# Optimization experiments

Measured on AMD Instinct MI355X. Metric: run time of the kernel, lower is better.

## Reference

```python
import jax, jax.numpy as jnp
import numpy as np

B, H, W, C, UNITS = 16, 64, 64, 64, 128

def setup_inputs() -> dict:
    key = jax.random.key(0)
    k1, k2 = jax.random.split(key)
    x = jax.random.normal(k1, (B, H, W, C), dtype=jnp.float32)
    # 'random_normal' keras initializer defaults to stddev=0.05
    w = jax.random.normal(k2, (UNITS, C, W, H), dtype=jnp.float32) * 0.05
    return {"x": x, "w": w}

def reference(x, w):
    # Original: transpose NHWC->NCHW, broadcasted matmul (W,H)@(H,W),
    # reduce-sum over C, transpose back, relu.
    # Fused contraction: y[b,i,j,u] = sum_{c,h} w[u,c,i,h] * x[b,h,j,c]
    y = jnp.einsum('ucih,bhjc->biju', w, x)  # (B, W, W, units)
    return jax.nn.relu(y)
```

## Files before the change

### kernel.cpp

```cpp
#include <hip/hip_runtime.h>
#include <hip/hip_bf16.h>


typedef __attribute__((ext_vector_type(4))) float f32x4;
typedef __attribute__((ext_vector_type(8))) short bf16x8;
typedef __attribute__((ext_vector_type(4))) unsigned int u32x4;
typedef __attribute__((ext_vector_type(2))) unsigned int u32x2;
typedef unsigned short ushort_t;

static __device__ __forceinline__ unsigned int cvt_pk_bf16(float lo, float hi) {
  unsigned int r;
  asm("v_cvt_pk_bf16_f32 %0, %1, %2" : "=v"(r) : "v"(lo), "v"(hi));
  return r;
}

static __device__ __forceinline__ void async_copy16(void* lds, const void* g) {
  __builtin_amdgcn_global_load_lds(
      (const __attribute__((address_space(1))) unsigned int*)g,
      (__attribute__((address_space(3))) unsigned int*)lds, 16, 0, 0);
}

__global__ __launch_bounds__(256)
void conv_x(const float* __restrict__ X, ushort_t* __restrict__ Xb, int n4) {
  int idx = blockIdx.x * 256 + threadIdx.x;
  const int stride = gridDim.x * 256;
  for (; idx < n4; idx += stride) {
    f32x4 v = ((const f32x4*)X)[idx];
    u32x2 o;
    o.x = cvt_pk_bf16(v.x, v.y);
    o.y = cvt_pk_bf16(v.z, v.w);
    ((u32x2*)Xb)[idx] = o;
  }
}

__global__ __launch_bounds__(256)
void conv_w(const float* __restrict__ W, ushort_t* __restrict__ Wb) {
  __shared__ float T[64][65];
  const int bid = blockIdx.x;
  const int u = bid >> 6;
  const int i = bid & 63;
  const int t = threadIdx.x;

  const int hq = t & 15;
  const int c4 = t >> 4;
  const float* base = W + (((size_t)u * 64) * 64 + i) * 64;
#pragma unroll
  for (int it = 0; it < 4; ++it) {
    const int c = it * 16 + c4;
    f32x4 v = *(const f32x4*)(base + (size_t)c * 4096 + hq * 4);
    *(f32x4*)&T[c][hq * 4] = v;
  }
  __syncthreads();

  const int h = t >> 2;
  const int c0 = (t & 3) * 16;
  unsigned int pk[8];
#pragma unroll
  for (int q = 0; q < 8; ++q)
    pk[q] = cvt_pk_bf16(T[c0 + 2 * q][h], T[c0 + 2 * q + 1][h]);
  ushort_t* out = Wb + (((size_t)i * 128 + u) * 64 + h) * 64 + c0;
  ((u32x4*)out)[0] = *(u32x4*)&pk[0];
  ((u32x4*)out)[1] = *(u32x4*)&pk[4];
}

__global__ __launch_bounds__(512, 2)
void gemm8(const ushort_t* __restrict__ Xb, const ushort_t* __restrict__ Wb,
           float* __restrict__ O) {
  __shared__ ushort_t As[3][128 * 64];
  __shared__ ushort_t Bs[3][256 * 64];

  const int tid = threadIdx.x;
  const int lane = tid & 63;
  const int wid = tid >> 6;
  const int wm = wid >> 2;
  const int wn = wid & 3;

  const int bid = blockIdx.x;
  const int wg = (bid & 7) * 32 + (bid >> 3);
  const int mt = wg & 7;
  const int nt2 = wg >> 3;

  const char* XbB = (const char*)Xb;
  const char* WbB = (const char*)Wb;

  int a_dst[2]; size_t a_src[2];
#pragma unroll
  for (int it = 0; it < 2; ++it) {
    const int flat = it * 8192 + tid * 16;
    const int row = flat >> 7;
    const int p = (flat >> 4) & 7;
    const int b = mt * 2 + (row >> 6);
    const int j = row & 63;
    a_dst[it] = flat;
    a_src[it] = (size_t)b * 524288 + (size_t)j * 128 + ((p ^ (row & 7)) << 4);
  }
  int b_dst[4]; size_t b_src[4];
#pragma unroll
  for (int it = 0; it < 4; ++it) {
    const int flat = it * 8192 + tid * 16;
    const int nl = flat >> 7;
    const int p = (flat >> 4) & 7;
    b_dst[it] = flat;
    b_src[it] = (size_t)(nt2 * 256 + nl) * 8192 + ((p ^ (nl & 7)) << 4);
  }

  int a_ro[2][4], b_ro[2][4];
#pragma unroll
  for (int kk = 0; kk < 2; ++kk) {
#pragma unroll
    for (int f = 0; f < 4; ++f) {
      int row = wm * 64 + f * 16 + (lane & 15);
      int byte0 = row * 128 + kk * 64 + (lane >> 4) * 16;
      a_ro[kk][f] = byte0 ^ ((row & 7) << 4);
      row = wn * 64 + f * 16 + (lane & 15);
      byte0 = row * 128 + kk * 64 + (lane >> 4) * 16;
      b_ro[kk][f] = byte0 ^ ((row & 7) << 4);
    }
  }

  f32x4 acc[4][4];
#pragma unroll
  for (int i = 0; i < 4; ++i)
#pragma unroll
    for (int j = 0; j < 4; ++j) acc[i][j] = (f32x4){0.f, 0.f, 0.f, 0.f};

  auto stage = [&](int buf, int h) {
    char* la = (char*)&As[buf][0];
    char* lb = (char*)&Bs[buf][0];
#pragma unroll
    for (int it = 0; it < 2; ++it)
      async_copy16(la + a_dst[it], XbB + a_src[it] + (size_t)h * 8192);
#pragma unroll
    for (int it = 0; it < 4; ++it)
      async_copy16(lb + b_dst[it], WbB + b_src[it] + (size_t)h * 128);
  };
  auto stage3a = [&](int buf, int h) {
    char* la = (char*)&As[buf][0];
    char* lb = (char*)&Bs[buf][0];
#pragma unroll
    for (int it = 0; it < 2; ++it)
      async_copy16(la + a_dst[it], XbB + a_src[it] + (size_t)h * 8192);
    async_copy16(lb + b_dst[0], WbB + b_src[0] + (size_t)h * 128);
  };
  auto stage3b = [&](int buf, int h) {
    char* lb = (char*)&Bs[buf][0];
#pragma unroll
    for (int it = 1; it < 4; ++it)
      async_copy16(lb + b_dst[it], WbB + b_src[it] + (size_t)h * 128);
  };

  bf16x8 fa0[4], fb0[4], fa1[4], fb1[4];

  auto readFrags = [&](bf16x8 (&fa)[4], bf16x8 (&fb)[4], int buf, int kk) {
    const char* ab = (const char*)&As[buf][0];
    const char* bb = (const char*)&Bs[buf][0];
#pragma unroll
    for (int f = 0; f < 4; ++f) fa[f] = *(const bf16x8*)(ab + a_ro[kk][f]);
#pragma unroll
    for (int f = 0; f < 4; ++f) fb[f] = *(const bf16x8*)(bb + b_ro[kk][f]);
  };

  stage(0, 0);
  stage(1, 1);
  asm volatile("s_waitcnt vmcnt(6)" ::: "memory");
  __builtin_amdgcn_s_barrier();
  readFrags(fa0, fb0, 0, 0);

  int cur = 0, nxt = 1, pre = 2;
  for (int t = 0; t < 64; ++t) {
    __builtin_amdgcn_sched_barrier(0);
    readFrags(fa1, fb1, cur, 1);
    if (t + 2 < 64) stage3a(pre, t + 2);
    if (t < 62) {
      asm volatile("s_waitcnt vmcnt(3)" ::: "memory");
    } else {
      asm volatile("s_waitcnt vmcnt(0)" ::: "memory");
    }
    __builtin_amdgcn_sched_barrier(0);
    __builtin_amdgcn_s_barrier();
    __builtin_amdgcn_s_setprio(1);
#pragma unroll
    for (int mf = 0; mf < 4; ++mf)
#pragma unroll
      for (int nf = 0; nf < 4; ++nf)
        acc[mf][nf] = __builtin_amdgcn_mfma_f32_16x16x32_bf16(
            fa0[mf], fb0[nf], acc[mf][nf], 0, 0, 0);
    __builtin_amdgcn_s_setprio(0);
    __builtin_amdgcn_s_barrier();

    __builtin_amdgcn_sched_barrier(0);
    if (t + 1 < 64) readFrags(fa0, fb0, nxt, 0);
    if (t + 2 < 64) stage3b(pre, t + 2);
    __builtin_amdgcn_sched_barrier(0);
    __builtin_amdgcn_s_barrier();
    __builtin_amdgcn_s_setprio(1);
#pragma unroll
    for (int mf = 0; mf < 4; ++mf)
#pragma unroll
      for (int nf = 0; nf < 4; ++nf)
        acc[mf][nf] = __builtin_amdgcn_mfma_f32_16x16x32_bf16(
            fa1[mf], fb1[nf], acc[mf][nf], 0, 0, 0);
    __builtin_amdgcn_s_setprio(0);
    __builtin_amdgcn_s_barrier();

    cur = (cur == 2) ? 0 : cur + 1;
    nxt = (nxt == 2) ? 0 : nxt + 1;
    pre = (pre == 2) ? 0 : pre + 1;
  }

  const int rbase = (lane >> 4) * 4;
  const int cn = lane & 15;
#pragma unroll
  for (int mf = 0; mf < 4; ++mf) {
#pragma unroll
    for (int r = 0; r < 4; ++r) {
      const int ml = wm * 64 + mf * 16 + rbase + r;
      const int m = mt * 128 + ml;
      const int b = m >> 6;
      const int j = m & 63;
#pragma unroll
      for (int nf = 0; nf < 4; ++nf) {
        const int nloc = wn * 64 + nf * 16 + cn;
        const int i = nt2 * 2 + (nloc >> 7);
        const int u = nloc & 127;
        O[(((size_t)b * 64 + i) * 64 + j) * 128 + u] = fmaxf(acc[mf][nf][r], 0.f);
      }
    }
  }
}

__global__ __launch_bounds__(256, 2)
void fused_gemm(const float* __restrict__ X, const float* __restrict__ Wt,
                float* __restrict__ O) {
  __shared__ ushort_t As[2][128 * 64];
  __shared__ ushort_t Bs[2][128 * 64];
  const int tid = threadIdx.x;
  const int lane = tid & 63;
  const int wid = tid >> 6;
  const int wm = wid >> 1;
  const int wn = wid & 1;
  const int bid = blockIdx.x;
  const int wg = (bid & 7) * 64 + (bid >> 3);
  const int mt = wg & 7;
  const int nt = wg >> 3;
  const int a_ml = tid >> 1;
  const int a_hp = (tid & 1) * 2;
  const int a_b = (mt * 128 + a_ml) >> 6;
  const int a_j = a_ml & 63;
  const float* a_base = X + ((size_t)a_b << 18) + ((size_t)a_j << 6);
  const int b_nl = tid >> 1;
  const int b_c8 = (tid & 1) * 8;
  const float* b_base = Wt + ((size_t)b_nl << 18) + ((size_t)nt << 6);
  f32x4 ra[2][4];
  f32x4 rb[8];
  f32x4 acc[4][4];
#pragma unroll
  for (int i = 0; i < 4; ++i)
#pragma unroll
    for (int j = 0; j < 4; ++j) acc[i][j] = (f32x4){0.f, 0.f, 0.f, 0.f};
  auto stage_load = [&](int t) {
    const int th = t & 15;
    const int tc = t >> 4;
    const int c0 = tc * 16;
    const int h0 = th * 4;
#pragma unroll
    for (int s = 0; s < 2; ++s) {
      const float* p = a_base + (size_t)(h0 + a_hp + s) * 4096 + c0;
#pragma unroll
      for (int q = 0; q < 4; ++q) ra[s][q] = ((const f32x4*)p)[q];
    }
#pragma unroll
    for (int q = 0; q < 8; ++q)
      rb[q] = *(const f32x4*)(b_base + (size_t)(c0 + b_c8 + q) * 4096 + h0);
  };
  auto stage_write = [&](int buf) {
    char* abase = (char*)&As[buf][0];
    const int swa = (a_ml & 7) << 4;
#pragma unroll
    for (int s = 0; s < 2; ++s) {
      u32x4 lo, hi;
      lo.x = cvt_pk_bf16(ra[s][0].x, ra[s][0].y);
      lo.y = cvt_pk_bf16(ra[s][0].z, ra[s][0].w);
      lo.z = cvt_pk_bf16(ra[s][1].x, ra[s][1].y);
      lo.w = cvt_pk_bf16(ra[s][1].z, ra[s][1].w);
      hi.x = cvt_pk_bf16(ra[s][2].x, ra[s][2].y);
      hi.y = cvt_pk_bf16(ra[s][2].z, ra[s][2].w);
      hi.z = cvt_pk_bf16(ra[s][3].x, ra[s][3].y);
      hi.w = cvt_pk_bf16(ra[s][3].z, ra[s][3].w);
      const int byte0 = a_ml * 128 + (a_hp + s) * 32;
      *(u32x4*)(abase + (byte0 ^ swa)) = lo;
      *(u32x4*)(abase + ((byte0 + 16) ^ swa)) = hi;
    }
    char* bbase = (char*)&Bs[buf][0];
    const int swb = (b_nl & 7) << 4;
#pragma unroll
    for (int hl = 0; hl < 4; ++hl) {
      u32x4 v;
      v.x = cvt_pk_bf16(rb[0][hl], rb[1][hl]);
      v.y = cvt_pk_bf16(rb[2][hl], rb[3][hl]);
      v.z = cvt_pk_bf16(rb[4][hl], rb[5][hl]);
      v.w = cvt_pk_bf16(rb[6][hl], rb[7][hl]);
      const int byte0 = b_nl * 128 + (hl * 16 + b_c8) * 2;
      *(u32x4*)(bbase + (byte0 ^ swb)) = v;
    }
  };
  auto compute = [&](int buf) {
    const char* abase = (const char*)&As[buf][0];
    const char* bbase = (const char*)&Bs[buf][0];
#pragma unroll
    for (int kk = 0; kk < 2; ++kk) {
      bf16x8 af[4], bfr[4];
#pragma unroll
      for (int mf = 0; mf < 4; ++mf) {
        const int row = wm * 64 + mf * 16 + (lane & 15);
        const int byte0 = row * 128 + kk * 64 + (lane >> 4) * 16;
        af[mf] = *(const bf16x8*)(abase + (byte0 ^ ((row & 7) << 4)));
      }
#pragma unroll
      for (int nf = 0; nf < 4; ++nf) {
        const int row = wn * 64 + nf * 16 + (lane & 15);
        const int byte0 = row * 128 + kk * 64 + (lane >> 4) * 16;
        bfr[nf] = *(const bf16x8*)(bbase + (byte0 ^ ((row & 7) << 4)));
      }
#pragma unroll
      for (int mf = 0; mf < 4; ++mf)
#pragma unroll
        for (int nf = 0; nf < 4; ++nf)
          acc[mf][nf] = __builtin_amdgcn_mfma_f32_16x16x32_bf16(
              af[mf], bfr[nf], acc[mf][nf], 0, 0, 0);
    }
  };
  stage_load(0);
  stage_write(0);
  __syncthreads();
  int cur = 0;
  for (int t = 0; t < 64; ++t) {
    if (t + 1 < 64) stage_load(t + 1);
    compute(cur);
    if (t + 1 < 64) stage_write(cur ^ 1);
    __syncthreads();
    cur ^= 1;
  }
  const int rbase = (lane >> 4) * 4;
  const int cn = lane & 15;
#pragma unroll
  for (int mf = 0; mf < 4; ++mf) {
#pragma unroll
    for (int r = 0; r < 4; ++r) {
      const int ml = wm * 64 + mf * 16 + rbase + r;
      const int m = mt * 128 + ml;
      const int b = m >> 6;
      const int j = m & 63;
      float* orow = O + (((size_t)b * 64 + nt) * 64 + j) * 128;
#pragma unroll
      for (int nf = 0; nf < 4; ++nf) {
        const int u = wn * 64 + nf * 16 + cn;
        orow[u] = fmaxf(acc[mf][nf][r], 0.f);
      }
    }
  }
}

extern "C" void kernel_launch(void* const* d_in, const int* in_sizes, int n_in,
                              void* d_out, int out_size, void* d_ws, size_t ws_size,
                              hipStream_t stream) {
  const float* x = (const float*)d_in[0];
  const float* w = (const float*)d_in[1];
  float* out = (float*)d_out;

  const size_t XB_BYTES = (size_t)16 * 64 * 64 * 64 * 2;
  const size_t WB_BYTES = (size_t)64 * 128 * 64 * 64 * 2;

  if (ws_size >= XB_BYTES + WB_BYTES) {
    ushort_t* Xb = (ushort_t*)d_ws;
    ushort_t* Wb = (ushort_t*)((char*)d_ws + XB_BYTES);
    hipLaunchKernelGGL(conv_x, dim3(1024), dim3(256), 0, stream, x, Xb,
                       (int)(16 * 64 * 64 * 64 / 4));
    hipLaunchKernelGGL(conv_w, dim3(8192), dim3(256), 0, stream, w, Wb);
    hipLaunchKernelGGL(gemm8, dim3(256), dim3(512), 0, stream, Xb, Wb, out);
  } else {
    hipLaunchKernelGGL(fused_gemm, dim3(512), dim3(256), 0, stream, x, w, out);
  }
}
```

Before: 107.1 us.

## Replace 8-wave GEMM with 4-wave 256x128 tile kernel using fewer barriers

The main GEMM now uses 256-thread blocks of 4 waves. Each wave computes a 128x64 output tile (8x4 MFMA fragments) instead of 64x64, and the block tile changes from 128x256 to 256x128. This doubles per-wave register reuse of B fragments and removes two of the four s_barriers per K iteration, cutting LDS traffic per MFMA and sync overhead. In exchange it uses more accumulator registers, gives one block per CU, and has fewer waves to hide latency. Removing barriers between reading a buffer and refilling it may also risk LDS hazards.

```diff
diff --git a/kernel.cpp b/kernel.cpp
--- a/kernel.cpp
+++ b/kernel.cpp
@@ -63,33 +63,33 @@
   ((u32x4*)out)[1] = *(u32x4*)&pk[4];
 }
 
-__global__ __launch_bounds__(512, 2)
-void gemm8(const ushort_t* __restrict__ Xb, const ushort_t* __restrict__ Wb,
-           float* __restrict__ O) {
-  __shared__ ushort_t As[3][128 * 64];
-  __shared__ ushort_t Bs[3][256 * 64];
+__global__ __launch_bounds__(256, 1)
+void gemm4f(const ushort_t* __restrict__ Xb, const ushort_t* __restrict__ Wb,
+            float* __restrict__ O) {
+  __shared__ ushort_t As[3][256 * 64];
+  __shared__ ushort_t Bs[3][128 * 64];
 
   const int tid = threadIdx.x;
   const int lane = tid & 63;
   const int wid = tid >> 6;
-  const int wm = wid >> 2;
-  const int wn = wid & 3;
+  const int wm = wid >> 1;
+  const int wn = wid & 1;
 
   const int bid = blockIdx.x;
   const int wg = (bid & 7) * 32 + (bid >> 3);
-  const int mt = wg & 7;
-  const int nt2 = wg >> 3;
+  const int mt = wg & 3;
+  const int nt = wg >> 2;
 
   const char* XbB = (const char*)Xb;
   const char* WbB = (const char*)Wb;
 
-  int a_dst[2]; size_t a_src[2];
-#pragma unroll
-  for (int it = 0; it < 2; ++it) {
-    const int flat = it * 8192 + tid * 16;
+  int a_dst[8]; size_t a_src[8];
+#pragma unroll
+  for (int it = 0; it < 8; ++it) {
+    const int flat = it * 4096 + tid * 16;
     const int row = flat >> 7;
     const int p = (flat >> 4) & 7;
-    const int b = mt * 2 + (row >> 6);
+    const int b = mt * 4 + (row >> 6);
     const int j = row & 63;
     a_dst[it] = flat;
     a_src[it] = (size_t)b * 524288 + (size_t)j * 128 + ((p ^ (row & 7)) << 4);
@@ -97,72 +97,63 @@
   int b_dst[4]; size_t b_src[4];
 #pragma unroll
   for (int it = 0; it < 4; ++it) {
-    const int flat = it * 8192 + tid * 16;
-    const int nl = flat >> 7;
+    const int flat = it * 4096 + tid * 16;
+    const int u = flat >> 7;
     const int p = (flat >> 4) & 7;
     b_dst[it] = flat;
-    b_src[it] = (size_t)(nt2 * 256 + nl) * 8192 + ((p ^ (nl & 7)) << 4);
-  }
-
-  int a_ro[2][4], b_ro[2][4];
+    b_src[it] = (size_t)(nt * 128 + u) * 8192 + ((p ^ (u & 7)) << 4);
+  }
+
+  int a_ro[2][8], b_ro[2][4];
 #pragma unroll
   for (int kk = 0; kk < 2; ++kk) {
 #pragma unroll
+    for (int f = 0; f < 8; ++f) {
+      const int row = wm * 128 + f * 16 + (lane & 15);
+      const int byte0 = row * 128 + kk * 64 + (lane >> 4) * 16;
+      a_ro[kk][f] = byte0 ^ ((row & 7) << 4);
+    }
+#pragma unroll
     for (int f = 0; f < 4; ++f) {
-      int row = wm * 64 + f * 16 + (lane & 15);
-      int byte0 = row * 128 + kk * 64 + (lane >> 4) * 16;
-      a_ro[kk][f] = byte0 ^ ((row & 7) << 4);
-      row = wn * 64 + f * 16 + (lane & 15);
-      byte0 = row * 128 + kk * 64 + (lane >> 4) * 16;
+      const int row = wn * 64 + f * 16 + (lane & 15);
+      const int byte0 = row * 128 + kk * 64 + (lane >> 4) * 16;
       b_ro[kk][f] = byte0 ^ ((row & 7) << 4);
     }
   }
 
-  f32x4 acc[4][4];
-#pragma unroll
-  for (int i = 0; i < 4; ++i)
+  f32x4 acc[8][4];
+#pragma unroll
+  for (int i = 0; i < 8; ++i)
 #pragma unroll
     for (int j = 0; j < 4; ++j) acc[i][j] = (f32x4){0.f, 0.f, 0.f, 0.f};
 
-  auto stage = [&](int buf, int h) {
+  auto stageA = [&](int buf, int h) {
     char* la = (char*)&As[buf][0];
+#pragma unroll
+    for (int it = 0; it < 8; ++it)
+      async_copy16(la + a_dst[it], XbB + a_src[it] + (size_t)h * 8192);
+  };
+  auto stageB = [&](int buf, int h) {
     char* lb = (char*)&Bs[buf][0];
-#pragma unroll
-    for (int it = 0; it < 2; ++it)
-      async_copy16(la + a_dst[it], XbB + a_src[it] + (size_t)h * 8192);
 #pragma unroll
     for (int it = 0; it < 4; ++it)
       async_copy16(lb + b_dst[it], WbB + b_src[it] + (size_t)h * 128);
   };
-  auto stage3a = [&](int buf, int h) {
-    char* la = (char*)&As[buf][0];
-    char* lb = (char*)&Bs[buf][0];
-#pragma unroll
-    for (int it = 0; it < 2; ++it)
-      async_copy16(la + a_dst[it], XbB + a_src[it] + (size_t)h * 8192);
-    async_copy16(lb + b_dst[0], WbB + b_src[0] + (size_t)h * 128);
-  };
-  auto stage3b = [&](int buf, int h) {
-    char* lb = (char*)&Bs[buf][0];
-#pragma unroll
-    for (int it = 1; it < 4; ++it)
-      async_copy16(lb + b_dst[it], WbB + b_src[it] + (size_t)h * 128);
-  };
-
-  bf16x8 fa0[4], fb0[4], fa1[4], fb1[4];
-
-  auto readFrags = [&](bf16x8 (&fa)[4], bf16x8 (&fb)[4], int buf, int kk) {
+
+  bf16x8 fa0[8], fb0[4], fa1[8], fb1[4];
+
+  auto readFrags = [&](bf16x8 (&fa)[8], bf16x8 (&fb)[4], int buf, int kk) {
     const char* ab = (const char*)&As[buf][0];
     const char* bb = (const char*)&Bs[buf][0];
 #pragma unroll
-    for (int f = 0; f < 4; ++f) fa[f] = *(const bf16x8*)(ab + a_ro[kk][f]);
+    for (int f = 0; f < 8; ++f) fa[f] = *(const bf16x8*)(ab + a_ro[kk][f]);
 #pragma unroll
     for (int f = 0; f < 4; ++f) fb[f] = *(const bf16x8*)(bb + b_ro[kk][f]);
   };
 
-  stage(0, 0);
-  stage(1, 1);
-  asm volatile("s_waitcnt vmcnt(6)" ::: "memory");
+  stageA(0, 0); stageB(0, 0);
+  stageA(1, 1); stageB(1, 1);
+  asm volatile("s_waitcnt vmcnt(12)" ::: "memory");
   __builtin_amdgcn_s_barrier();
   readFrags(fa0, fb0, 0, 0);
 
@@ -170,9 +161,9 @@
   for (int t = 0; t < 64; ++t) {
     __builtin_amdgcn_sched_barrier(0);
     readFrags(fa1, fb1, cur, 1);
-    if (t + 2 < 64) stage3a(pre, t + 2);
+    if (t + 2 < 64) stageA(pre, t + 2);
     if (t < 62) {
-      asm volatile("s_waitcnt vmcnt(3)" ::: "memory");
+      asm volatile("s_waitcnt vmcnt(8)" ::: "memory");
     } else {
       asm volatile("s_waitcnt vmcnt(0)" ::: "memory");
     }
@@ -180,22 +171,19 @@
     __builtin_amdgcn_s_barrier();
     __builtin_amdgcn_s_setprio(1);
 #pragma unroll
-    for (int mf = 0; mf < 4; ++mf)
+    for (int mf = 0; mf < 8; ++mf)
 #pragma unroll
       for (int nf = 0; nf < 4; ++nf)
         acc[mf][nf] = __builtin_amdgcn_mfma_f32_16x16x32_bf16(
             fa0[mf], fb0[nf], acc[mf][nf], 0, 0, 0);
     __builtin_amdgcn_s_setprio(0);
-    __builtin_amdgcn_s_barrier();
 
     __builtin_amdgcn_sched_barrier(0);
     if (t + 1 < 64) readFrags(fa0, fb0, nxt, 0);
-    if (t + 2 < 64) stage3b(pre, t + 2);
-    __builtin_amdgcn_sched_barrier(0);
-    __builtin_amdgcn_s_barrier();
+    if (t + 2 < 64) stageB(pre, t + 2);
     __builtin_amdgcn_s_setprio(1);
 #pragma unroll
-    for (int mf = 0; mf < 4; ++mf)
+    for (int mf = 0; mf < 8; ++mf)
 #pragma unroll
       for (int nf = 0; nf < 4; ++nf)
         acc[mf][nf] = __builtin_amdgcn_mfma_f32_16x16x32_bf16(
@@ -211,19 +199,18 @@
   const int rbase = (lane >> 4) * 4;
   const int cn = lane & 15;
 #pragma unroll
-  for (int mf = 0; mf < 4; ++mf) {
+  for (int mf = 0; mf < 8; ++mf) {
 #pragma unroll
     for (int r = 0; r < 4; ++r) {
-      const int ml = wm * 64 + mf * 16 + rbase + r;
-      const int m = mt * 128 + ml;
+      const int ml = wm * 128 + mf * 16 + rbase + r;
+      const int m = mt * 256 + ml;
       const int b = m >> 6;
       const int j = m & 63;
+      float* orow = O + (((size_t)b * 64 + nt) * 64 + j) * 128;
 #pragma unroll
       for (int nf = 0; nf < 4; ++nf) {
-        const int nloc = wn * 64 + nf * 16 + cn;
-        const int i = nt2 * 2 + (nloc >> 7);
-        const int u = nloc & 127;
-        O[(((size_t)b * 64 + i) * 64 + j) * 128 + u] = fmaxf(acc[mf][nf][r], 0.f);
+        const int u = wn * 64 + nf * 16 + cn;
+        orow[u] = fmaxf(acc[mf][nf][r], 0.f);
       }
     }
   }
@@ -377,7 +364,7 @@
     hipLaunchKernelGGL(conv_x, dim3(1024), dim3(256), 0, stream, x, Xb,
                        (int)(16 * 64 * 64 * 64 / 4));
     hipLaunchKernelGGL(conv_w, dim3(8192), dim3(256), 0, stream, w, Wb);
-    hipLaunchKernelGGL(gemm8, dim3(256), dim3(512), 0, stream, Xb, Wb, out);
+    hipLaunchKernelGGL(gemm4f, dim3(256), dim3(256), 0, stream, Xb, Wb, out);
   } else {
     hipLaunchKernelGGL(fused_gemm, dim3(512), dim3(256), 0, stream, x, w, out);
   }
```

Result: slower. 148.0 us (+38.2%).

## Add split-K 256x256-tile GEMM with partial buffers and separate add+ReLU pass

Applied to the files above, without the earlier changes.

Adds a new GEMM kernel with 256x256 output tiles that splits the K dimension (h) in two, so each of the 256 workgroups handles half the reduction. The two halves go to the output buffer and a workspace buffer, and a separate add_relu kernel then sums them and applies ReLU. The larger tile raises operand reuse per LDS byte, and the K split keeps enough workgroups in flight. In exchange the fp32 partial result is written twice and read back, which adds memory traffic, an extra launch, and a larger workspace requirement.

```diff
diff --git a/kernel.cpp b/kernel.cpp
--- a/kernel.cpp
+++ b/kernel.cpp
@@ -63,6 +63,172 @@
   ((u32x4*)out)[1] = *(u32x4*)&pk[4];
 }
 
+__global__ __launch_bounds__(512, 1)
+void gemm256(const ushort_t* __restrict__ Xb, const ushort_t* __restrict__ Wb,
+             float* __restrict__ P0, float* __restrict__ P1) {
+  __shared__ ushort_t As[3][256 * 32];
+  __shared__ ushort_t Bs[3][256 * 32];
+
+  const int tid = threadIdx.x;
+  const int lane = tid & 63;
+  const int wid = tid >> 6;
+  const int wm = wid >> 2;
+  const int wn = wid & 3;
+
+  const int bid = blockIdx.x;
+  const int wg = (bid & 7) * 32 + (bid >> 3);
+  const int mt = wg & 3;
+  const int rest = wg >> 2;
+  const int ks = rest & 1;
+  const int nt2 = rest >> 1;
+
+  const char* XbB = (const char*)Xb;
+  const char* WbB = (const char*)Wb;
+  const int kb6 = ks * 32;
+
+  int a_dst[2]; size_t a_srcb[2];
+  int b_dst[2]; size_t b_srcb[2];
+#pragma unroll
+  for (int it = 0; it < 2; ++it) {
+    const int flat = it * 8192 + tid * 16;
+    const int row = flat >> 6;
+    const int p = (flat >> 4) & 3;
+    const int ps = p ^ ((row >> 1) & 3);
+    a_dst[it] = flat;
+    a_srcb[it] = (size_t)(mt * 4 + (row >> 6)) * 524288 +
+                 (size_t)(row & 63) * 128 + ps * 16;
+    b_dst[it] = flat;
+    b_srcb[it] = (size_t)(nt2 * 256 + row) * 8192 + ps * 16;
+  }
+
+  int a_ro[2][4], b_ro[4];
+#pragma unroll
+  for (int mh = 0; mh < 2; ++mh)
+#pragma unroll
+    for (int f = 0; f < 4; ++f) {
+      const int row = wm * 128 + mh * 64 + f * 16 + (lane & 15);
+      a_ro[mh][f] = row * 64 + (((lane >> 4) ^ ((row >> 1) & 3)) << 4);
+    }
+#pragma unroll
+  for (int f = 0; f < 4; ++f) {
+    const int row = wn * 64 + f * 16 + (lane & 15);
+    b_ro[f] = row * 64 + (((lane >> 4) ^ ((row >> 1) & 3)) << 4);
+  }
+
+  f32x4 acc[8][4];
+#pragma unroll
+  for (int i = 0; i < 8; ++i)
+#pragma unroll
+    for (int j = 0; j < 4; ++j) acc[i][j] = (f32x4){0.f, 0.f, 0.f, 0.f};
+
+  auto stageA = [&](int buf, int T) {
+    char* la = (char*)&As[buf][0];
+    const size_t koff = (size_t)(kb6 + (T >> 1)) * 8192 + (T & 1) * 64;
+#pragma unroll
+    for (int it = 0; it < 2; ++it)
+      async_copy16(la + a_dst[it], XbB + a_srcb[it] + koff);
+  };
+  auto stageB = [&](int buf, int T) {
+    char* lb = (char*)&Bs[buf][0];
+    const size_t koff = (size_t)(kb6 + (T >> 1)) * 128 + (T & 1) * 64;
+#pragma unroll
+    for (int it = 0; it < 2; ++it)
+      async_copy16(lb + b_dst[it], WbB + b_srcb[it] + koff);
+  };
+
+  stageA(0, 0); stageB(0, 0);
+  stageA(1, 1); stageB(1, 1);
+  asm volatile("s_waitcnt vmcnt(4)" ::: "memory");
+  __builtin_amdgcn_s_barrier();
+
+  int cur = 0, pre = 2;
+  for (int t = 0; t < 64; ++t) {
+    const char* ab = (const char*)&As[cur][0];
+    const char* bb = (const char*)&Bs[cur][0];
+    bf16x8 fa[4], fb[4], fa2[4];
+
+    __builtin_amdgcn_sched_barrier(0);
+#pragma unroll
+    for (int f = 0; f < 4; ++f) fa[f] = *(const bf16x8*)(ab + a_ro[0][f]);
+#pragma unroll
+    for (int f = 0; f < 4; ++f) fb[f] = *(const bf16x8*)(bb + b_ro[f]);
+    if (t + 2 < 64) stageA(pre, t + 2);
+    __builtin_amdgcn_s_barrier();
+    asm volatile("s_waitcnt lgkmcnt(0)" ::: "memory");
+    __builtin_amdgcn_sched_barrier(0);
+    __builtin_amdgcn_s_setprio(1);
+#pragma unroll
+    for (int f = 0; f < 4; ++f)
+#pragma unroll
+      for (int nf = 0; nf < 4; ++nf)
+        acc[f][nf] = __builtin_amdgcn_mfma_f32_16x16x32_bf16(
+            fa[f], fb[nf], acc[f][nf], 0, 0, 0);
+    __builtin_amdgcn_s_setprio(0);
+    __builtin_amdgcn_s_barrier();
+
+    __builtin_amdgcn_sched_barrier(0);
+#pragma unroll
+    for (int f = 0; f < 4; ++f) fa2[f] = *(const bf16x8*)(ab + a_ro[1][f]);
+    if (t + 2 < 64) stageB(pre, t + 2);
+    __builtin_amdgcn_s_barrier();
+    asm volatile("s_waitcnt lgkmcnt(0)" ::: "memory");
+    __builtin_amdgcn_sched_barrier(0);
+    __builtin_amdgcn_s_setprio(1);
+#pragma unroll
+    for (int f = 0; f < 4; ++f)
+#pragma unroll
+      for (int nf = 0; nf < 4; ++nf)
+        acc[4 + f][nf] = __builtin_amdgcn_mfma_f32_16x16x32_bf16(
+            fa2[f], fb[nf], acc[4 + f][nf], 0, 0, 0);
+    __builtin_amdgcn_s_setprio(0);
+    if (t < 62) {
+      asm volatile("s_waitcnt vmcnt(4)" ::: "memory");
+    } else if (t == 62) {
+      asm volatile("s_waitcnt vmcnt(0)" ::: "memory");
+    }
+    __builtin_amdgcn_s_barrier();
+
+    cur = (cur == 2) ? 0 : cur + 1;
+    pre = (pre == 2) ? 0 : pre + 1;
+  }
+
+  float* P = ks ? P1 : P0;
+  const int rbase = (lane >> 4) * 4;
+  const int cn = lane & 15;
+#pragma unroll
+  for (int mf = 0; mf < 8; ++mf) {
+#pragma unroll
+    for (int r = 0; r < 4; ++r) {
+      const int m = mt * 256 + wm * 128 + mf * 16 + rbase + r;
+      const int b = m >> 6;
+      const int j = m & 63;
+#pragma unroll
+      for (int nf = 0; nf < 4; ++nf) {
+        const int nloc = wn * 64 + nf * 16 + cn;
+        const int i = nt2 * 2 + (nloc >> 7);
+        const int u = nloc & 127;
+        P[(((size_t)b * 64 + i) * 64 + j) * 128 + u] = acc[mf][nf][r];
+      }
+    }
+  }
+}
+
+__global__ __launch_bounds__(256)
+void add_relu(float* __restrict__ Out, const float* __restrict__ P1, int n4) {
+  int idx = blockIdx.x * 256 + threadIdx.x;
+  const int stride = gridDim.x * 256;
+  for (; idx < n4; idx += stride) {
+    f32x4 a = ((const f32x4*)Out)[idx];
+    f32x4 b = ((const f32x4*)P1)[idx];
+    f32x4 r;
+    r.x = fmaxf(a.x + b.x, 0.f);
+    r.y = fmaxf(a.y + b.y, 0.f);
+    r.z = fmaxf(a.z + b.z, 0.f);
+    r.w = fmaxf(a.w + b.w, 0.f);
+    ((f32x4*)Out)[idx] = r;
+  }
+}
+
 __global__ __launch_bounds__(512, 2)
 void gemm8(const ushort_t* __restrict__ Xb, const ushort_t* __restrict__ Wb,
            float* __restrict__ O) {
@@ -150,7 +316,6 @@
   };
 
   bf16x8 fa0[4], fb0[4], fa1[4], fb1[4];
-
   auto readFrags = [&](bf16x8 (&fa)[4], bf16x8 (&fb)[4], int buf, int kk) {
     const char* ab = (const char*)&As[buf][0];
     const char* bb = (const char*)&Bs[buf][0];
@@ -370,8 +535,19 @@
 
   const size_t XB_BYTES = (size_t)16 * 64 * 64 * 64 * 2;
   const size_t WB_BYTES = (size_t)64 * 128 * 64 * 64 * 2;
-
-  if (ws_size >= XB_BYTES + WB_BYTES) {
+  const size_t P1_BYTES = (size_t)16 * 64 * 64 * 128 * 4;
+
+  if (ws_size >= XB_BYTES + WB_BYTES + P1_BYTES) {
+    ushort_t* Xb = (ushort_t*)d_ws;
+    ushort_t* Wb = (ushort_t*)((char*)d_ws + XB_BYTES);
+    float* P1 = (float*)((char*)d_ws + XB_BYTES + WB_BYTES);
+    hipLaunchKernelGGL(conv_x, dim3(1024), dim3(256), 0, stream, x, Xb,
+                       (int)(16 * 64 * 64 * 64 / 4));
+    hipLaunchKernelGGL(conv_w, dim3(8192), dim3(256), 0, stream, w, Wb);
+    hipLaunchKernelGGL(gemm256, dim3(256), dim3(512), 0, stream, Xb, Wb, out, P1);
+    hipLaunchKernelGGL(add_relu, dim3(2048), dim3(256), 0, stream, out, P1,
+                       (int)(16 * 64 * 64 * 128 / 4));
+  } else if (ws_size >= XB_BYTES + WB_BYTES) {
     ushort_t* Xb = (ushort_t*)d_ws;
     ushort_t* Wb = (ushort_t*)((char*)d_ws + XB_BYTES);
     hipLaunchKernelGGL(conv_x, dim3(1024), dim3(256), 0, stream, x, Xb,
```

After: 132.0 us. 23.2% more time.

## Fuse weight bf16 conversion into GEMM and transpose X to k-contiguous layout

Applied to the files above, without the earlier changes.

Removes the separate conv_w pre-pass. The GEMM now loads fp32 weights straight from global memory into registers, converts them to bf16 and writes them into LDS one stage ahead, with a software pipeline across two register sets. conv_x becomes a transpose kernel that lays X out so the GEMM's k dimension is contiguous. This avoids writing and re-reading a full bf16 copy of W, at the cost of register-staged loads instead of async LDS copies, extra VGPR pressure (launch bounds drop to one block per CU), and strided 32-byte fp32 reads of W.

```diff
diff --git a/kernel.cpp b/kernel.cpp
--- a/kernel.cpp
+++ b/kernel.cpp
@@ -5,7 +5,6 @@
 typedef __attribute__((ext_vector_type(4))) float f32x4;
 typedef __attribute__((ext_vector_type(8))) short bf16x8;
 typedef __attribute__((ext_vector_type(4))) unsigned int u32x4;
-typedef __attribute__((ext_vector_type(2))) unsigned int u32x2;
 typedef unsigned short ushort_t;
 
 static __device__ __forceinline__ unsigned int cvt_pk_bf16(float lo, float hi) {
@@ -21,51 +20,40 @@
 }
 
 __global__ __launch_bounds__(256)
-void conv_x(const float* __restrict__ X, ushort_t* __restrict__ Xb, int n4) {
-  int idx = blockIdx.x * 256 + threadIdx.x;
-  const int stride = gridDim.x * 256;
-  for (; idx < n4; idx += stride) {
-    f32x4 v = ((const f32x4*)X)[idx];
-    u32x2 o;
-    o.x = cvt_pk_bf16(v.x, v.y);
-    o.y = cvt_pk_bf16(v.z, v.w);
-    ((u32x2*)Xb)[idx] = o;
-  }
-}
-
-__global__ __launch_bounds__(256)
-void conv_w(const float* __restrict__ W, ushort_t* __restrict__ Wb) {
-  __shared__ float T[64][65];
+void conv_xT(const float* __restrict__ X, ushort_t* __restrict__ Xb) {
+  __shared__ float T[64][68];
   const int bid = blockIdx.x;
-  const int u = bid >> 6;
-  const int i = bid & 63;
+  const int b = bid >> 6;
+  const int j = bid & 63;
   const int t = threadIdx.x;
 
-  const int hq = t & 15;
-  const int c4 = t >> 4;
-  const float* base = W + (((size_t)u * 64) * 64 + i) * 64;
-#pragma unroll
-  for (int it = 0; it < 4; ++it) {
-    const int c = it * 16 + c4;
-    f32x4 v = *(const f32x4*)(base + (size_t)c * 4096 + hq * 4);
-    *(f32x4*)&T[c][hq * 4] = v;
+  {
+    const int h = t >> 2;
+    const int cq = (t & 3) * 16;
+    const float* src = X + (((size_t)(b * 64 + h) * 64 + j) * 64) + cq;
+#pragma unroll
+    for (int k = 0; k < 4; ++k) {
+      f32x4 v = ((const f32x4*)src)[k];
+      *(f32x4*)&T[h][cq + 4 * k] = v;
+    }
   }
   __syncthreads();
-
-  const int h = t >> 2;
-  const int c0 = (t & 3) * 16;
-  unsigned int pk[8];
-#pragma unroll
-  for (int q = 0; q < 8; ++q)
-    pk[q] = cvt_pk_bf16(T[c0 + 2 * q][h], T[c0 + 2 * q + 1][h]);
-  ushort_t* out = Wb + (((size_t)i * 128 + u) * 64 + h) * 64 + c0;
-  ((u32x4*)out)[0] = *(u32x4*)&pk[0];
-  ((u32x4*)out)[1] = *(u32x4*)&pk[4];
-}
-
-__global__ __launch_bounds__(512, 2)
-void gemm8(const ushort_t* __restrict__ Xb, const ushort_t* __restrict__ Wb,
-           float* __restrict__ O) {
+  {
+    const int c = t >> 2;
+    const int hq = (t & 3) * 16;
+    unsigned int pk[8];
+#pragma unroll
+    for (int k = 0; k < 8; ++k)
+      pk[k] = cvt_pk_bf16(T[hq + 2 * k][c], T[hq + 2 * k + 1][c]);
+    ushort_t* out = Xb + ((size_t)bid * 64 + c) * 64 + hq;
+    ((u32x4*)out)[0] = *(u32x4*)&pk[0];
+    ((u32x4*)out)[1] = *(u32x4*)&pk[4];
+  }
+}
+
+__global__ __launch_bounds__(512, 1)
+void gemm_fw(const ushort_t* __restrict__ Xb, const float* __restrict__ W,
+             float* __restrict__ O) {
   __shared__ ushort_t As[3][128 * 64];
   __shared__ ushort_t Bs[3][256 * 64];
 
@@ -81,27 +69,30 @@
   const int nt2 = wg >> 3;
 
   const char* XbB = (const char*)Xb;
-  const char* WbB = (const char*)Wb;
-
-  int a_dst[2]; size_t a_src[2];
+  const char* WB = (const char*)W;
+
+  int a_dst[2]; size_t a_gsrc[2];
 #pragma unroll
   for (int it = 0; it < 2; ++it) {
     const int flat = it * 8192 + tid * 16;
-    const int row = flat >> 7;
+    const int ml = flat >> 7;
     const int p = (flat >> 4) & 7;
-    const int b = mt * 2 + (row >> 6);
-    const int j = row & 63;
+    const int ps = p ^ (ml & 7);
     a_dst[it] = flat;
-    a_src[it] = (size_t)b * 524288 + (size_t)j * 128 + ((p ^ (row & 7)) << 4);
-  }
-  int b_dst[4]; size_t b_src[4];
-#pragma unroll
-  for (int it = 0; it < 4; ++it) {
-    const int flat = it * 8192 + tid * 16;
+    a_gsrc[it] = (size_t)(mt * 128 + ml) * 8192 + ps * 16;
+  }
+
+  int b_ldst[4]; size_t b_gsrc[4];
+#pragma unroll
+  for (int q = 0; q < 4; ++q) {
+    const int flat = q * 8192 + tid * 16;
     const int nl = flat >> 7;
     const int p = (flat >> 4) & 7;
-    b_dst[it] = flat;
-    b_src[it] = (size_t)(nt2 * 256 + nl) * 8192 + ((p ^ (nl & 7)) << 4);
+    const int ps = p ^ (nl & 7);
+    const int u = nl & 127;
+    const int il = nl >> 7;
+    b_ldst[q] = flat;
+    b_gsrc[q] = (size_t)u * 1048576 + (size_t)(nt2 * 2 + il) * 256 + ps * 32;
   }
 
   int a_ro[2][4], b_ro[2][4];
@@ -124,33 +115,34 @@
 #pragma unroll
     for (int j = 0; j < 4; ++j) acc[i][j] = (f32x4){0.f, 0.f, 0.f, 0.f};
 
-  auto stage = [&](int buf, int h) {
+  auto issueA = [&](int buf, int c) {
     char* la = (char*)&As[buf][0];
+#pragma unroll
+    for (int it = 0; it < 2; ++it)
+      async_copy16(la + a_dst[it], XbB + a_gsrc[it] + (size_t)c * 128);
+  };
+  auto issueB = [&](f32x4 (&r)[4][2], int c) {
+#pragma unroll
+    for (int q = 0; q < 4; ++q) {
+      const char* s = WB + b_gsrc[q] + (size_t)c * 16384;
+      r[q][0] = *(const f32x4*)s;
+      r[q][1] = *(const f32x4*)(s + 16);
+    }
+  };
+  auto cvtWriteB = [&](f32x4 (&r)[4][2], int buf) {
     char* lb = (char*)&Bs[buf][0];
 #pragma unroll
-    for (int it = 0; it < 2; ++it)
-      async_copy16(la + a_dst[it], XbB + a_src[it] + (size_t)h * 8192);
-#pragma unroll
-    for (int it = 0; it < 4; ++it)
-      async_copy16(lb + b_dst[it], WbB + b_src[it] + (size_t)h * 128);
-  };
-  auto stage3a = [&](int buf, int h) {
-    char* la = (char*)&As[buf][0];
-    char* lb = (char*)&Bs[buf][0];
-#pragma unroll
-    for (int it = 0; it < 2; ++it)
-      async_copy16(la + a_dst[it], XbB + a_src[it] + (size_t)h * 8192);
-    async_copy16(lb + b_dst[0], WbB + b_src[0] + (size_t)h * 128);
-  };
-  auto stage3b = [&](int buf, int h) {
-    char* lb = (char*)&Bs[buf][0];
-#pragma unroll
-    for (int it = 1; it < 4; ++it)
-      async_copy16(lb + b_dst[it], WbB + b_src[it] + (size_t)h * 128);
+    for (int q = 0; q < 4; ++q) {
+      u32x4 v;
+      v.x = cvt_pk_bf16(r[q][0].x, r[q][0].y);
+      v.y = cvt_pk_bf16(r[q][0].z, r[q][0].w);
+      v.z = cvt_pk_bf16(r[q][1].x, r[q][1].y);
+      v.w = cvt_pk_bf16(r[q][1].z, r[q][1].w);
+      *(u32x4*)(lb + b_ldst[q]) = v;
+    }
   };
 
   bf16x8 fa0[4], fb0[4], fa1[4], fb1[4];
-
   auto readFrags = [&](bf16x8 (&fa)[4], bf16x8 (&fb)[4], int buf, int kk) {
     const char* ab = (const char*)&As[buf][0];
     const char* bb = (const char*)&Bs[buf][0];
@@ -160,23 +152,21 @@
     for (int f = 0; f < 4; ++f) fb[f] = *(const bf16x8*)(bb + b_ro[kk][f]);
   };
 
-  stage(0, 0);
-  stage(1, 1);
-  asm volatile("s_waitcnt vmcnt(6)" ::: "memory");
-  __builtin_amdgcn_s_barrier();
-  readFrags(fa0, fb0, 0, 0);
-
+  f32x4 rB0[4][2], rB1[4][2];
   int cur = 0, nxt = 1, pre = 2;
-  for (int t = 0; t < 64; ++t) {
+
+  auto step = [&](int t, f32x4 (&rStage)[4][2], f32x4 (&rOther)[4][2]) {
     __builtin_amdgcn_sched_barrier(0);
     readFrags(fa1, fb1, cur, 1);
-    if (t + 2 < 64) stage3a(pre, t + 2);
+    if (t + 2 < 64) { issueB(rOther, t + 2); issueA(pre, t + 2); }
     if (t < 62) {
-      asm volatile("s_waitcnt vmcnt(3)" ::: "memory");
+      asm volatile("s_waitcnt vmcnt(10)" ::: "memory");
     } else {
       asm volatile("s_waitcnt vmcnt(0)" ::: "memory");
     }
+    if (t + 1 < 64) cvtWriteB(rStage, nxt);
     __builtin_amdgcn_sched_barrier(0);
+    asm volatile("s_waitcnt lgkmcnt(0)" ::: "memory");
     __builtin_amdgcn_s_barrier();
     __builtin_amdgcn_s_setprio(1);
 #pragma unroll
@@ -190,7 +180,6 @@
 
     __builtin_amdgcn_sched_barrier(0);
     if (t + 1 < 64) readFrags(fa0, fb0, nxt, 0);
-    if (t + 2 < 64) stage3b(pre, t + 2);
     __builtin_amdgcn_sched_barrier(0);
     __builtin_amdgcn_s_barrier();
     __builtin_amdgcn_s_setprio(1);
@@ -206,6 +195,19 @@
     cur = (cur == 2) ? 0 : cur + 1;
     nxt = (nxt == 2) ? 0 : nxt + 1;
     pre = (pre == 2) ? 0 : pre + 1;
+  };
+
+  issueB(rB0, 0); issueA(0, 0);
+  issueB(rB1, 1); issueA(1, 1);
+  asm volatile("s_waitcnt vmcnt(10)" ::: "memory");
+  cvtWriteB(rB0, 0);
+  asm volatile("s_waitcnt lgkmcnt(0)" ::: "memory");
+  __builtin_amdgcn_s_barrier();
+  readFrags(fa0, fb0, 0, 0);
+
+  for (int t = 0; t < 64; t += 2) {
+    step(t, rB1, rB0);
+    step(t + 1, rB0, rB1);
   }
 
   const int rbase = (lane >> 4) * 4;
@@ -369,15 +371,11 @@
   float* out = (float*)d_out;
 
   const size_t XB_BYTES = (size_t)16 * 64 * 64 * 64 * 2;
-  const size_t WB_BYTES = (size_t)64 * 128 * 64 * 64 * 2;
-
-  if (ws_size >= XB_BYTES + WB_BYTES) {
+
+  if (ws_size >= XB_BYTES) {
     ushort_t* Xb = (ushort_t*)d_ws;
-    ushort_t* Wb = (ushort_t*)((char*)d_ws + XB_BYTES);
-    hipLaunchKernelGGL(conv_x, dim3(1024), dim3(256), 0, stream, x, Xb,
-                       (int)(16 * 64 * 64 * 64 / 4));
-    hipLaunchKernelGGL(conv_w, dim3(8192), dim3(256), 0, stream, w, Wb);
-    hipLaunchKernelGGL(gemm8, dim3(256), dim3(512), 0, stream, Xb, Wb, out);
+    hipLaunchKernelGGL(conv_xT, dim3(1024), dim3(256), 0, stream, x, Xb);
+    hipLaunchKernelGGL(gemm_fw, dim3(256), dim3(512), 0, stream, Xb, w, out);
   } else {
     hipLaunchKernelGGL(fused_gemm, dim3(512), dim3(256), 0, stream, x, w, out);
   }
```

Result: slower. 118.9 us (+11.0%).
